# Optimization experiments

Measured on AMD Instinct MI355X. Metric: run time of the kernel, lower is better.

## Reference

```python
import jax, jax.numpy as jnp
import numpy as np

N = 40000      # total nodes in batched graph
E = 400000     # total edges
IN = 256       # input feature dim (n_dim / in_feats)
OUT = 256      # out_feats (DGL GatedGraphConv requires in_feats <= out_feats)
B = 256        # number of graphs in the batch
STEPS = 3      # GRU propagation steps per GatedGraphConv layer


def _gru_cell(m, h, Wih, Whh, bih, bhh):
    # torch.nn.GRUCell math
    gi = m @ Wih.T + bih          # [N, 3*OUT]
    gh = h @ Whh.T + bhh
    ir, iz, inn = jnp.split(gi, 3, axis=-1)
    hr, hz, hn = jnp.split(gh, 3, axis=-1)
    r = jax.nn.sigmoid(ir + hr)
    z = jax.nn.sigmoid(iz + hz)
    n = jnp.tanh(inn + r * hn)
    return (1.0 - z) * n + z * h


def _gated_graph_conv(h, src, dst, W, b, Wih, Whh, bih, bhh):
    # DGL GatedGraphConv with n_etypes=1: zero-pad to out_feats, then
    # n_steps of (per-etype linear -> sum messages over edges -> GRU update)
    if h.shape[1] < OUT:
        h = jnp.pad(h, ((0, 0), (0, OUT - h.shape[1])))
    for _ in range(STEPS):
        a = h @ W.T + b                                      # [N, OUT]
        m = jax.ops.segment_sum(a[src], dst, num_segments=N)  # gather/scatter
        h = _gru_cell(m, h, Wih, Whh, bih, bhh)
    return h


def _global_attention_pool(h, graph_ids, Wg, bg):
    gate = h @ Wg.T + bg                                       # [N, 1]
    gmax = jax.ops.segment_max(gate, graph_ids, num_segments=B)  # [B, 1]
    e = jnp.exp(gate - gmax[graph_ids])
    denom = jax.ops.segment_sum(e, graph_ids, num_segments=B)
    alpha = e / denom[graph_ids]                               # per-graph softmax
    return jax.ops.segment_sum(h * alpha, graph_ids, num_segments=B)  # [B, OUT]


def _forward(features, W0, b0, Wih0, Whh0, bih0, bhh0,
             W1, b1, Wih1, Whh1, bih1, bhh1, Wg, bg, Wo, bo,
             src, dst, graph_ids):
    # forward(): y = sigmoid(layer0(g, x)); y = sigmoid(layer1(g, y));
    # y = attention_pool(g, y); return sigmoid(output_layer(y))  (BCE branch)
    y = jax.nn.sigmoid(_gated_graph_conv(features, src, dst, W0, b0, Wih0, Whh0, bih0, bhh0))
    y = jax.nn.sigmoid(_gated_graph_conv(y, src, dst, W1, b1, Wih1, Whh1, bih1, bhh1))
    y = _global_attention_pool(y, graph_ids, Wg, bg)           # [B, OUT]
    return jax.nn.sigmoid(y @ Wo.T + bo)                        # [B, 1]


def setup_inputs() -> dict:
    key = jax.random.key(0)
    ks = jax.random.split(key, 20)
    s = lambda k, shape: (jax.random.normal(k, shape, jnp.float32) * 0.05)
    inp = {}
    inp["features"] = jax.random.normal(ks[0], (N, IN), jnp.float32)
    inp["src"] = jax.random.randint(ks[1], (E,), 0, N, jnp.int32)
    inp["dst"] = jax.random.randint(ks[2], (E,), 0, N, jnp.int32)
    inp["graph_ids"] = jnp.sort(jax.random.randint(ks[3], (N,), 0, B, jnp.int32))
    for li, off in ((0, 4), (1, 8)):
        inp[f"W{li}"] = s(ks[off], (OUT, OUT))
        inp[f"b{li}"] = jnp.zeros((OUT,), jnp.float32)
        inp[f"Wih{li}"] = s(ks[off + 1], (3 * OUT, OUT))
        inp[f"Whh{li}"] = s(ks[off + 2], (3 * OUT, OUT))
        inp[f"bih{li}"] = jnp.zeros((3 * OUT,), jnp.float32)
        inp[f"bhh{li}"] = jnp.zeros((3 * OUT,), jnp.float32)
    inp["Wg"] = s(ks[16], (1, OUT))
    inp["bg"] = jnp.zeros((1,), jnp.float32)
    inp["Wo"] = s(ks[17], (1, OUT))
    inp["bo"] = jnp.zeros((1,), jnp.float32)
    return inp


def reference(features, src, dst, graph_ids,
              W0, b0, Wih0, Whh0, bih0, bhh0,
              W1, b1, Wih1, Whh1, bih1, bhh1,
              Wg, bg, Wo, bo):
    return _forward(features, W0, b0, Wih0, Whh0, bih0, bhh0,
                    W1, b1, Wih1, Whh1, bih1, bhh1, Wg, bg, Wo, bo,
                    src, dst, graph_ids)
```

## Files before the change

### kernel.cpp

```cpp
#include <hip/hip_runtime.h>
#include <math.h>

#define NN 40000
#define EE 400000
#define BB 256

typedef __attribute__((ext_vector_type(8))) short short8;
typedef __attribute__((ext_vector_type(4))) float f32x4;
typedef __attribute__((address_space(1))) unsigned int glb_u32;
typedef __attribute__((address_space(3))) unsigned int lds_u32;

#define MFMA16 __builtin_amdgcn_mfma_f32_16x16x32_bf16

__device__ __forceinline__ float sigf(float x) { return 1.0f / (1.0f + __expf(-x)); }
__device__ __forceinline__ float tanhfast(float x) { return 2.0f / (1.0f + __expf(-2.0f * x)) - 1.0f; }
__device__ __forceinline__ unsigned short f2b(float f) {
    unsigned u = __float_as_uint(f);
    u += 0x7FFFu + ((u >> 16) & 1u);
    return (unsigned short)(u >> 16);
}
__device__ __forceinline__ float b2f(unsigned short h) { return __uint_as_float(((unsigned)h) << 16); }
__device__ __forceinline__ short8 ld8(const unsigned short* p) {
    return __builtin_bit_cast(short8, *(const uint4*)p);
}
__device__ __forceinline__ void gld_lds16(const void* g, void* l) {
    __builtin_amdgcn_global_load_lds((const glb_u32*)g, (lds_u32*)l, 16, 0, 0);
}

__global__ void k_f2b(const float* __restrict__ s, unsigned short* __restrict__ d, int n4) {
    int i = blockIdx.x * blockDim.x + threadIdx.x;
    if (i < n4) {
        float4 v = ((const float4*)s)[i];
        ushort4 o;
        o.x = f2b(v.x); o.y = f2b(v.y); o.z = f2b(v.z); o.w = f2b(v.w);
        ((ushort4*)d)[i] = o;
    }
}

__global__ __launch_bounds__(256) void k_wfuse(const float* __restrict__ Wih,
                                               const float* __restrict__ W,
                                               const float* __restrict__ b,
                                               unsigned short* __restrict__ Wf,
                                               float* __restrict__ vib) {
    int g = blockIdx.x;
    int c = threadIdx.x;
    __shared__ float row[256];
    __shared__ float red[256];
    row[c] = Wih[(size_t)g * 256 + c];
    __syncthreads();
    float acc = 0.f;
#pragma unroll 8
    for (int o = 0; o < 256; o++) acc += row[o] * W[(size_t)o * 256 + c];
    Wf[(size_t)g * 256 + c] = f2b(acc);
    red[c] = row[c] * b[c];
    __syncthreads();
    for (int off = 128; off; off >>= 1) {
        if (c < off) red[c] += red[c + off];
        __syncthreads();
    }
    if (c == 0) vib[g] = red[0];
}

__global__ void k_wpack(const unsigned short* __restrict__ Wf,
                        const float* __restrict__ Whh,
                        unsigned short* __restrict__ Wp) {
    int id = blockIdx.x * 256 + threadIdx.x;
    if (id >= 49152) return;
    int lane = id & 63;
    int t = (id >> 6) & 3;
    int q = (id >> 8) % 6;
    int bk = (id >> 8) / 6;
    int ks = bk & 7, bn_t = bk >> 3;
    int col = bn_t * 64 + t * 16 + (lane & 15);
    int k = ks * 32 + (lane >> 4) * 8;
    unsigned short o[8];
    if (q < 3) {
        const unsigned short* s = Wf + (size_t)(q * 256 + col) * 256 + k;
#pragma unroll
        for (int j = 0; j < 8; j++) o[j] = s[j];
    } else {
        const float* s = Whh + (size_t)((q - 3) * 256 + col) * 256 + k;
#pragma unroll
        for (int j = 0; j < 8; j++) o[j] = f2b(s[j]);
    }
    *(uint4*)(Wp + (size_t)id * 8) = *(const uint4*)o;
}

__global__ void k_zeroi(int* __restrict__ p, int n) {
    int i = blockIdx.x * blockDim.x + threadIdx.x;
    if (i < n) p[i] = 0;
}

__global__ void k_hist(const int* __restrict__ dst, int* __restrict__ cnt) {
    int e = blockIdx.x * blockDim.x + threadIdx.x;
    if (e < EE) atomicAdd(&cnt[dst[e]], 1);
}

__global__ __launch_bounds__(1024) void k_scanA(const int* __restrict__ cnt, int* __restrict__ rp,
                                                int* __restrict__ bsum) {
    __shared__ int sm[1024];
    int b = blockIdx.x, t = threadIdx.x;
    int i = b * 1024 + t;
    sm[t] = (i < NN) ? cnt[i] : 0;
    __syncthreads();
    for (int off = 1; off < 1024; off <<= 1) {
        int u = (t >= off) ? sm[t - off] : 0;
        __syncthreads();
        sm[t] += u;
        __syncthreads();
    }
    if (i < NN) rp[i + 1] = sm[t];
    if (t == 1023) bsum[b] = sm[1023];
}

__global__ void k_scanB(const int* __restrict__ bsum, int* __restrict__ boff, int* __restrict__ rp) {
    if (threadIdx.x == 0) {
        int run = 0;
        for (int k = 0; k < 40; k++) { boff[k] = run; run += bsum[k]; }
        rp[0] = 0;
    }
}

__global__ void k_scanC(int* __restrict__ rp, const int* __restrict__ boff) {
    int i = blockIdx.x * 256 + threadIdx.x;
    if (i < NN) rp[i + 1] += boff[i >> 10];
}

__global__ void k_fill(const int* __restrict__ src, const int* __restrict__ dst,
                       const int* __restrict__ rp, int* __restrict__ cur, int* __restrict__ cs) {
    int e = blockIdx.x * blockDim.x + threadIdx.x;
    if (e < EE) {
        int v = dst[e];
        int pos = rp[v] + atomicAdd(&cur[v], 1);
        cs[pos] = src[e];
    }
}

__device__ __forceinline__ void acc8(float* a, uint4 v) {
    a[0] += b2f((unsigned short)(v.x & 0xFFFF));
    a[1] += b2f((unsigned short)(v.x >> 16));
    a[2] += b2f((unsigned short)(v.y & 0xFFFF));
    a[3] += b2f((unsigned short)(v.y >> 16));
    a[4] += b2f((unsigned short)(v.z & 0xFFFF));
    a[5] += b2f((unsigned short)(v.z >> 16));
    a[6] += b2f((unsigned short)(v.w & 0xFFFF));
    a[7] += b2f((unsigned short)(v.w >> 16));
}

__global__ __launch_bounds__(256) void k_aggr(const unsigned short* __restrict__ Hb,
                                              const int* __restrict__ rp,
                                              const int* __restrict__ cs,
                                              unsigned short* __restrict__ Agg) {
    int v = blockIdx.x * 8 + (threadIdx.x >> 5);
    int hl = threadIdx.x & 31;
    int s = rp[v], e = rp[v + 1];
    float a[8] = {};
    int j = s;
    for (; j + 8 <= e; j += 8) {
        uint4 x0 = *(const uint4*)&Hb[(size_t)cs[j] * 256 + hl * 8];
        uint4 x1 = *(const uint4*)&Hb[(size_t)cs[j + 1] * 256 + hl * 8];
        uint4 x2 = *(const uint4*)&Hb[(size_t)cs[j + 2] * 256 + hl * 8];
        uint4 x3 = *(const uint4*)&Hb[(size_t)cs[j + 3] * 256 + hl * 8];
        uint4 x4 = *(const uint4*)&Hb[(size_t)cs[j + 4] * 256 + hl * 8];
        uint4 x5 = *(const uint4*)&Hb[(size_t)cs[j + 5] * 256 + hl * 8];
        uint4 x6 = *(const uint4*)&Hb[(size_t)cs[j + 6] * 256 + hl * 8];
        uint4 x7 = *(const uint4*)&Hb[(size_t)cs[j + 7] * 256 + hl * 8];
        acc8(a, x0); acc8(a, x1); acc8(a, x2); acc8(a, x3);
        acc8(a, x4); acc8(a, x5); acc8(a, x6); acc8(a, x7);
    }
    for (; j < e; j++) {
        uint4 x = *(const uint4*)&Hb[(size_t)cs[j] * 256 + hl * 8];
        acc8(a, x);
    }
    uint4 o;
    o.x = (unsigned)f2b(a[0]) | ((unsigned)f2b(a[1]) << 16);
    o.y = (unsigned)f2b(a[2]) | ((unsigned)f2b(a[3]) << 16);
    o.z = (unsigned)f2b(a[4]) | ((unsigned)f2b(a[5]) << 16);
    o.w = (unsigned)f2b(a[6]) | ((unsigned)f2b(a[7]) << 16);
    *(uint4*)&Agg[(size_t)v * 256 + hl * 8] = o;
}

__global__ __launch_bounds__(256, 3) void k_gru(const unsigned short* __restrict__ Mb,
                                                const unsigned short* __restrict__ Hb,
                                                const char* __restrict__ Wp,
                                                const float* __restrict__ bih,
                                                const float* __restrict__ bhh,
                                                const float* __restrict__ vib,
                                                const int* __restrict__ cnt,
                                                unsigned short* __restrict__ Hout, int fin) {
    __shared__ uint4 Wl[2][1536];
    const int tid = threadIdx.x;
    const int lane = tid & 63, wid = tid >> 6;
    const int wr = wid >> 1, wc = wid & 1;
    const int p = blockIdx.x;
    const int xcd = p & 7, rank = p >> 3;
    const int logical = (xcd < 4 ? xcd * 313 : 1252 + (xcd - 4) * 312) + rank;
    const int bm = (logical >> 2) * 64, bn_t = logical & 3, bn = bn_t * 64;
    const int l15 = lane & 15, lk = lane >> 4;

    const unsigned short* m0p = Mb + (size_t)(bm + wr * 32 + l15) * 256 + lk * 8;
    const unsigned short* m1p = m0p + 16 * 256;
    const unsigned short* h0p = Hb + (size_t)(bm + wr * 32 + l15) * 256 + lk * 8;
    const unsigned short* h1p = h0p + 16 * 256;

    const char* wbase = Wp + (size_t)bn_t * 8 * 24576;
    char* lds0 = (char*)&Wl[0][0];
    char* lds1 = (char*)&Wl[1][0];
    const int soff = wid * 1024 + lane * 16;

#define STAGE(b, ks)                                                        \
    {                                                                       \
        const char* gs = wbase + (ks) * 24576;                              \
        char* lb = (b) ? lds1 : lds0;                                       \
        _Pragma("unroll") for (int i = 0; i < 6; i++)                       \
            gld_lds16(gs + i * 4096 + soff, lb + i * 4096 + wid * 1024);    \
    }

    f32x4 acc[6][2][2] = {};
    short8 m0, m1, h0, h1, nm0, nm1, nh0, nh1;

    STAGE(0, 0);
    asm volatile("" ::: "memory");
    m0 = ld8(m0p); m1 = ld8(m1p); h0 = ld8(h0p); h1 = ld8(h1p);

    for (int ks = 0; ks < 8; ks++) {
        int cur = ks & 1;
        asm volatile("s_waitcnt vmcnt(4)" ::: "memory");
        __builtin_amdgcn_s_barrier();
        __builtin_amdgcn_sched_barrier(0);
        if (ks < 7) {
            STAGE(cur ^ 1, ks + 1);
            asm volatile("" ::: "memory");
            int ke = (ks + 1) * 32;
            nm0 = ld8(m0p + ke); nm1 = ld8(m1p + ke);
            nh0 = ld8(h0p + ke); nh1 = ld8(h1p + ke);
        }
        __builtin_amdgcn_s_setprio(1);
#pragma unroll
        for (int q = 0; q < 6; q++) {
            short8 b0 = __builtin_bit_cast(short8, Wl[cur][(q * 4 + wc * 2 + 0) * 64 + lane]);
            short8 b1 = __builtin_bit_cast(short8, Wl[cur][(q * 4 + wc * 2 + 1) * 64 + lane]);
            short8 a0 = q < 3 ? m0 : h0;
            short8 a1 = q < 3 ? m1 : h1;
            acc[q][0][0] = MFMA16(a0, b0, acc[q][0][0], 0, 0, 0);
            acc[q][1][0] = MFMA16(a1, b0, acc[q][1][0], 0, 0, 0);
            acc[q][0][1] = MFMA16(a0, b1, acc[q][0][1], 0, 0, 0);
            acc[q][1][1] = MFMA16(a1, b1, acc[q][1][1], 0, 0, 0);
        }
        __builtin_amdgcn_s_setprio(0);
        m0 = nm0; m1 = nm1; h0 = nh0; h1 = nh1;
    }
#undef STAGE

    const int lk4 = lk * 4;
#pragma unroll
    for (int f = 0; f < 2; f++)
#pragma unroll
        for (int t = 0; t < 2; t++) {
            int col = bn + wc * 32 + t * 16 + l15;
            float bi0 = bih[col], bi1 = bih[col + 256], bi2 = bih[col + 512];
            float bh0 = bhh[col], bh1 = bhh[col + 256], bh2 = bhh[col + 512];
            float v0 = vib[col], v1 = vib[col + 256], v2 = vib[col + 512];
#pragma unroll
            for (int r = 0; r < 4; r++) {
                int n = bm + wr * 32 + f * 16 + lk4 + r;
                float cf = (float)cnt[n];
                float ho = b2f(Hb[(size_t)n * 256 + col]);
                float irv = acc[0][f][t][r] + bi0 + cf * v0;
                float izv = acc[1][f][t][r] + bi1 + cf * v1;
                float inv = acc[2][f][t][r] + bi2 + cf * v2;
                float hrv = acc[3][f][t][r] + bh0;
                float hzv = acc[4][f][t][r] + bh1;
                float hnv = acc[5][f][t][r] + bh2;
                float rg = sigf(irv + hrv);
                float zg = sigf(izv + hzv);
                float nv = tanhfast(inv + rg * hnv);
                float v = (1.0f - zg) * nv + zg * ho;
                if (fin) v = sigf(v);
                Hout[(size_t)n * 256 + col] = f2b(v);
            }
        }
}

__global__ __launch_bounds__(256) void k_gate(const unsigned short* __restrict__ H,
                                              const float* __restrict__ Wg,
                                              const float* __restrict__ bg,
                                              float* __restrict__ gate) {
    int v = blockIdx.x * 4 + (threadIdx.x >> 6);
    int lane = threadIdx.x & 63;
    if (v >= NN) return;
    ushort4 hv = *(const ushort4*)&H[(size_t)v * 256 + lane * 4];
    float4 wv = *(const float4*)&Wg[lane * 4];
    float s = b2f(hv.x) * wv.x + b2f(hv.y) * wv.y + b2f(hv.z) * wv.z + b2f(hv.w) * wv.w;
    for (int off = 32; off; off >>= 1) s += __shfl_down(s, off);
    if (lane == 0) gate[v] = s + bg[0];
}

__global__ void k_bounds(const int* __restrict__ ids, int* __restrict__ gs, int* __restrict__ ge) {
    int b = threadIdx.x;
    int lo = 0, hi = NN;
    while (lo < hi) { int mid = (lo + hi) >> 1; if (ids[mid] < b) lo = mid + 1; else hi = mid; }
    gs[b] = lo;
    lo = 0; hi = NN;
    int key = b + 1;
    while (lo < hi) { int mid = (lo + hi) >> 1; if (ids[mid] < key) lo = mid + 1; else hi = mid; }
    ge[b] = lo;
}

__global__ __launch_bounds__(256) void k_pool(const unsigned short* __restrict__ H,
                                              const float* __restrict__ gate,
                                              const int* __restrict__ gs,
                                              const int* __restrict__ ge,
                                              float* __restrict__ pooled) {
    int b = blockIdx.x;
    int s = gs[b], e = ge[b];
    int t = threadIdx.x;
    __shared__ float red[256];
    __shared__ float wsh[256];
    float mx = -INFINITY;
    for (int n = s + t; n < e; n += 256) mx = fmaxf(mx, gate[n]);
    red[t] = mx;
    __syncthreads();
    for (int off = 128; off; off >>= 1) {
        if (t < off) red[t] = fmaxf(red[t], red[t + off]);
        __syncthreads();
    }
    mx = red[0];
    __syncthreads();
    float sm = 0.f;
    for (int n = s + t; n < e; n += 256) sm += __expf(gate[n] - mx);
    red[t] = sm;
    __syncthreads();
    for (int off = 128; off; off >>= 1) {
        if (t < off) red[t] += red[t + off];
        __syncthreads();
    }
    float denom = red[0];
    __syncthreads();
    float acc = 0.f;
    for (int c = s; c < e; c += 256) {
        int n = c + t;
        wsh[t] = (n < e) ? __expf(gate[n] - mx) / denom : 0.f;
        __syncthreads();
        int lim = e - c; if (lim > 256) lim = 256;
        for (int q = 0; q < lim; q++) acc += wsh[q] * b2f(H[(size_t)(c + q) * 256 + t]);
        __syncthreads();
    }
    pooled[(size_t)b * 256 + t] = acc;
}

__global__ void k_out(const float* __restrict__ pooled, const float* __restrict__ Wo,
                      const float* __restrict__ bo, float* __restrict__ out) {
    int b = blockIdx.x;
    int lane = threadIdx.x;
    float4 pv = *(const float4*)&pooled[(size_t)b * 256 + lane * 4];
    float4 wv = *(const float4*)&Wo[lane * 4];
    float s = pv.x * wv.x + pv.y * wv.y + pv.z * wv.z + pv.w * wv.w;
    for (int off = 32; off; off >>= 1) s += __shfl_down(s, off);
    if (lane == 0) out[b] = sigf(s + bo[0]);
}

extern "C" void kernel_launch(void* const* d_in, const int* in_sizes, int n_in,
                              void* d_out, int out_size, void* d_ws, size_t ws_size,
                              hipStream_t stream) {
    const float* features = (const float*)d_in[0];
    const int* src = (const int*)d_in[1];
    const int* dst = (const int*)d_in[2];
    const int* gids = (const int*)d_in[3];
    const float* W[2]   = {(const float*)d_in[4],  (const float*)d_in[10]};
    const float* bW[2]  = {(const float*)d_in[5],  (const float*)d_in[11]};
    const float* Wih[2] = {(const float*)d_in[6],  (const float*)d_in[12]};
    const float* Whh[2] = {(const float*)d_in[7],  (const float*)d_in[13]};
    const float* bih[2] = {(const float*)d_in[8],  (const float*)d_in[14]};
    const float* bhh[2] = {(const float*)d_in[9],  (const float*)d_in[15]};
    const float* Wg = (const float*)d_in[16];
    const float* bg = (const float*)d_in[17];
    const float* Wo = (const float*)d_in[18];
    const float* bo = (const float*)d_in[19];
    float* out = (float*)d_out;

    char* p = (char*)d_ws;
    auto alloc = [&](size_t bytes) {
        char* r = p;
        p += (bytes + 255) / 256 * 256;
        return r;
    };
    unsigned short* hbF = (unsigned short*)alloc((size_t)NN * 256 * 2);
    unsigned short* hA = (unsigned short*)alloc((size_t)NN * 256 * 2);
    unsigned short* hB = (unsigned short*)alloc((size_t)NN * 256 * 2);
    unsigned short* agg = (unsigned short*)alloc((size_t)NN * 256 * 2);
    unsigned short* Wfb[2], *Wpk[2];
    float* vib[2];
    for (int i = 0; i < 2; i++) {
        Wfb[i] = (unsigned short*)alloc((size_t)768 * 256 * 2);
        Wpk[i] = (unsigned short*)alloc((size_t)49152 * 16);
        vib[i] = (float*)alloc((size_t)768 * 4);
    }
    int* rp = (int*)alloc((size_t)(NN + 1) * 4);
    int* cnt = (int*)alloc((size_t)NN * 4);
    int* cur = (int*)alloc((size_t)NN * 4);
    int* cs = (int*)alloc((size_t)EE * 4);
    int* bsum = (int*)alloc(64 * 4);
    int* boff = (int*)alloc(64 * 4);
    float* gate = (float*)alloc((size_t)NN * 4);
    int* gsb = (int*)alloc((size_t)BB * 4);
    int* geb = (int*)alloc((size_t)BB * 4);
    float* pooled = (float*)alloc((size_t)BB * 256 * 4);

    k_f2b<<<(NN * 256 / 4 + 255) / 256, 256, 0, stream>>>(features, hbF, NN * 256 / 4);
    for (int i = 0; i < 2; i++) {
        k_wfuse<<<768, 256, 0, stream>>>(Wih[i], W[i], bW[i], Wfb[i], vib[i]);
        k_wpack<<<192, 256, 0, stream>>>(Wfb[i], Whh[i], Wpk[i]);
    }

    k_zeroi<<<(NN + 255) / 256, 256, 0, stream>>>(cnt, NN);
    k_zeroi<<<(NN + 255) / 256, 256, 0, stream>>>(cur, NN);
    k_hist<<<(EE + 255) / 256, 256, 0, stream>>>(dst, cnt);
    k_scanA<<<40, 1024, 0, stream>>>(cnt, rp, bsum);
    k_scanB<<<1, 64, 0, stream>>>(bsum, boff, rp);
    k_scanC<<<157, 256, 0, stream>>>(rp, boff);
    k_fill<<<(EE + 255) / 256, 256, 0, stream>>>(src, dst, rp, cur, cs);
    k_bounds<<<1, 256, 0, stream>>>(gids, gsb, geb);

    const unsigned short* hcur = hbF;
    unsigned short* hnext = hA;
    for (int li = 0; li < 2; li++) {
        for (int s = 0; s < 3; s++) {
            k_aggr<<<5000, 256, 0, stream>>>(hcur, rp, cs, agg);
            int fin = (s == 2) ? 1 : 0;
            k_gru<<<2500, 256, 0, stream>>>(agg, hcur, (const char*)Wpk[li], bih[li], bhh[li],
                                            vib[li], cnt, hnext, fin);
            hcur = hnext;
            hnext = (hnext == hA) ? hB : hA;
        }
    }
    k_gate<<<10000, 256, 0, stream>>>(hcur, Wg, bg, gate);
    k_pool<<<BB, 256, 0, stream>>>(hcur, gate, gsb, geb, pooled);
    k_out<<<BB, 64, 0, stream>>>(pooled, Wo, bo, out);
}
```

Baseline: 720.6 us.

## Triple-buffer GRU weight staging with two-stage-ahead prefetch

Converts the k_gru K-loop from a double-buffered to a triple-buffered pipeline. Weight tiles and M/H activation fragments are prefetched two k-steps ahead, with the vmcnt waits adjusted to match. The loop is fully unrolled so the register arrays index statically. This is meant to hide more global-load latency, but it raises LDS use per block to 72KB and lowers the launch-bounds occupancy hint from 3 to 2 blocks per CU.

```diff
diff --git a/kernel.cpp b/kernel.cpp
--- a/kernel.cpp
+++ b/kernel.cpp
@@ -180,7 +180,7 @@
     *(uint4*)&Agg[(size_t)v * 256 + hl * 8] = o;
 }
 
-__global__ __launch_bounds__(256, 3) void k_gru(const unsigned short* __restrict__ Mb,
+__global__ __launch_bounds__(256, 2) void k_gru(const unsigned short* __restrict__ Mb,
                                                 const unsigned short* __restrict__ Hb,
                                                 const char* __restrict__ Wp,
                                                 const float* __restrict__ bih,
@@ -188,7 +188,7 @@
                                                 const float* __restrict__ vib,
                                                 const int* __restrict__ cnt,
                                                 unsigned short* __restrict__ Hout, int fin) {
-    __shared__ uint4 Wl[2][1536];
+    __shared__ uint4 Wl[3][1536];
     const int tid = threadIdx.x;
     const int lane = tid & 63, wid = tid >> 6;
     const int wr = wid >> 1, wc = wid & 1;
@@ -204,51 +204,58 @@
     const unsigned short* h1p = h0p + 16 * 256;
 
     const char* wbase = Wp + (size_t)bn_t * 8 * 24576;
-    char* lds0 = (char*)&Wl[0][0];
-    char* lds1 = (char*)&Wl[1][0];
+    char* ldsb = (char*)&Wl[0][0];
     const int soff = wid * 1024 + lane * 16;
 
-#define STAGE(b, ks)                                                        \
+#define STAGE(bi, ks)                                                       \
     {                                                                       \
         const char* gs = wbase + (ks) * 24576;                              \
-        char* lb = (b) ? lds1 : lds0;                                       \
+        char* lb = ldsb + (bi) * 24576;                                     \
         _Pragma("unroll") for (int i = 0; i < 6; i++)                       \
             gld_lds16(gs + i * 4096 + soff, lb + i * 4096 + wid * 1024);    \
     }
 
     f32x4 acc[6][2][2] = {};
-    short8 m0, m1, h0, h1, nm0, nm1, nh0, nh1;
+    short8 m0[3], m1[3], h0[3], h1[3];
 
     STAGE(0, 0);
     asm volatile("" ::: "memory");
-    m0 = ld8(m0p); m1 = ld8(m1p); h0 = ld8(h0p); h1 = ld8(h1p);
-
+    m0[0] = ld8(m0p); m1[0] = ld8(m1p); h0[0] = ld8(h0p); h1[0] = ld8(h1p);
+    asm volatile("" ::: "memory");
+    STAGE(1, 1);
+    asm volatile("" ::: "memory");
+    m0[1] = ld8(m0p + 32); m1[1] = ld8(m1p + 32);
+    h0[1] = ld8(h0p + 32); h1[1] = ld8(h1p + 32);
+
+#pragma unroll
     for (int ks = 0; ks < 8; ks++) {
-        int cur = ks & 1;
-        asm volatile("s_waitcnt vmcnt(4)" ::: "memory");
+        const int cur = ks % 3;
+        if (ks < 7) asm volatile("s_waitcnt vmcnt(14)" ::: "memory");
+        else        asm volatile("s_waitcnt vmcnt(4)" ::: "memory");
         __builtin_amdgcn_s_barrier();
         __builtin_amdgcn_sched_barrier(0);
-        if (ks < 7) {
-            STAGE(cur ^ 1, ks + 1);
+        if (ks < 6) {
+            const int sl = (ks + 2) % 3;
+            STAGE(sl, ks + 2);
             asm volatile("" ::: "memory");
-            int ke = (ks + 1) * 32;
-            nm0 = ld8(m0p + ke); nm1 = ld8(m1p + ke);
-            nh0 = ld8(h0p + ke); nh1 = ld8(h1p + ke);
+            const int ke = (ks + 2) * 32;
+            m0[sl] = ld8(m0p + ke); m1[sl] = ld8(m1p + ke);
+            h0[sl] = ld8(h0p + ke); h1[sl] = ld8(h1p + ke);
+            asm volatile("" ::: "memory");
         }
         __builtin_amdgcn_s_setprio(1);
 #pragma unroll
         for (int q = 0; q < 6; q++) {
             short8 b0 = __builtin_bit_cast(short8, Wl[cur][(q * 4 + wc * 2 + 0) * 64 + lane]);
             short8 b1 = __builtin_bit_cast(short8, Wl[cur][(q * 4 + wc * 2 + 1) * 64 + lane]);
-            short8 a0 = q < 3 ? m0 : h0;
-            short8 a1 = q < 3 ? m1 : h1;
+            short8 a0 = q < 3 ? m0[cur] : h0[cur];
+            short8 a1 = q < 3 ? m1[cur] : h1[cur];
             acc[q][0][0] = MFMA16(a0, b0, acc[q][0][0], 0, 0, 0);
             acc[q][1][0] = MFMA16(a1, b0, acc[q][1][0], 0, 0, 0);
             acc[q][0][1] = MFMA16(a0, b1, acc[q][0][1], 0, 0, 0);
             acc[q][1][1] = MFMA16(a1, b1, acc[q][1][1], 0, 0, 0);
         }
         __builtin_amdgcn_s_setprio(0);
-        m0 = nm0; m1 = nm1; h0 = nh0; h1 = nh1;
     }
 #undef STAGE
 
```

Measured after the change: 768.1 us. +6.6%, slower.

## Halve GRU kernel column tile to 32 and double grid for higher occupancy

Applied to the files above, without the earlier changes.

The fused GRU GEMM kernel now computes a 64x32 output tile per block instead of 64x64. This halves the accumulators and the LDS weight staging buffer, raises launch bounds to 6 blocks per SM, and doubles the grid to 5000 blocks. The block-to-XCD remapping is simplified to match. The aim is more resident waves to hide memory latency, at the cost of loading the M and H A-operands twice as often across blocks.

```diff
diff --git a/kernel.cpp b/kernel.cpp
--- a/kernel.cpp
+++ b/kernel.cpp
@@ -180,7 +180,7 @@
     *(uint4*)&Agg[(size_t)v * 256 + hl * 8] = o;
 }
 
-__global__ __launch_bounds__(256, 3) void k_gru(const unsigned short* __restrict__ Mb,
+__global__ __launch_bounds__(256, 6) void k_gru(const unsigned short* __restrict__ Mb,
                                                 const unsigned short* __restrict__ Hb,
                                                 const char* __restrict__ Wp,
                                                 const float* __restrict__ bih,
@@ -188,14 +188,15 @@
                                                 const float* __restrict__ vib,
                                                 const int* __restrict__ cnt,
                                                 unsigned short* __restrict__ Hout, int fin) {
-    __shared__ uint4 Wl[2][1536];
+    __shared__ uint4 Wl[2][768];
     const int tid = threadIdx.x;
     const int lane = tid & 63, wid = tid >> 6;
     const int wr = wid >> 1, wc = wid & 1;
     const int p = blockIdx.x;
-    const int xcd = p & 7, rank = p >> 3;
-    const int logical = (xcd < 4 ? xcd * 313 : 1252 + (xcd - 4) * 312) + rank;
-    const int bm = (logical >> 2) * 64, bn_t = logical & 3, bn = bn_t * 64;
+    const int logical = (p & 7) * 625 + (p >> 3);
+    const int rowtile = logical >> 3, bn32 = logical & 7;
+    const int bm = rowtile * 64;
+    const int bn_t = bn32 >> 1, hw = bn32 & 1;
     const int l15 = lane & 15, lk = lane >> 4;
 
     const unsigned short* m0p = Mb + (size_t)(bm + wr * 32 + l15) * 256 + lk * 8;
@@ -203,83 +204,80 @@
     const unsigned short* h0p = Hb + (size_t)(bm + wr * 32 + l15) * 256 + lk * 8;
     const unsigned short* h1p = h0p + 16 * 256;
 
-    const char* wbase = Wp + (size_t)bn_t * 8 * 24576;
+    const char* wbase = Wp + (size_t)bn_t * 196608 + hw * 2048 + lane * 16;
     char* lds0 = (char*)&Wl[0][0];
-    char* lds1 = (char*)&Wl[1][0];
-    const int soff = wid * 1024 + lane * 16;
-
-#define STAGE(b, ks)                                                        \
-    {                                                                       \
-        const char* gs = wbase + (ks) * 24576;                              \
-        char* lb = (b) ? lds1 : lds0;                                       \
-        _Pragma("unroll") for (int i = 0; i < 6; i++)                       \
-            gld_lds16(gs + i * 4096 + soff, lb + i * 4096 + wid * 1024);    \
-    }
-
-    f32x4 acc[6][2][2] = {};
-    short8 m0, m1, h0, h1, nm0, nm1, nh0, nh1;
+
+#define STAGE(b, ks)                                                          \
+    {                                                                         \
+        const char* gs = wbase + (ks) * 24576;                                \
+        char* lb = lds0 + (b) * 12288;                                        \
+        _Pragma("unroll") for (int i = 0; i < 3; i++) {                       \
+            int f = wid * 3 + i;                                              \
+            gld_lds16(gs + (f >> 1) * 4096 + (f & 1) * 1024, lb + f * 1024);  \
+        }                                                                     \
+    }
+
+    f32x4 acc[6][2] = {};
+    short8 am0, am1, ah0, ah1, nm0, nm1, nh0, nh1;
 
     STAGE(0, 0);
     asm volatile("" ::: "memory");
-    m0 = ld8(m0p); m1 = ld8(m1p); h0 = ld8(h0p); h1 = ld8(h1p);
-
+    am0 = ld8(m0p); am1 = ld8(m1p); ah0 = ld8(h0p); ah1 = ld8(h1p);
+
+#pragma unroll
     for (int ks = 0; ks < 8; ks++) {
-        int cur = ks & 1;
+        const int cur = ks & 1;
         asm volatile("s_waitcnt vmcnt(4)" ::: "memory");
         __builtin_amdgcn_s_barrier();
         __builtin_amdgcn_sched_barrier(0);
         if (ks < 7) {
             STAGE(cur ^ 1, ks + 1);
             asm volatile("" ::: "memory");
-            int ke = (ks + 1) * 32;
+            const int ke = (ks + 1) * 32;
             nm0 = ld8(m0p + ke); nm1 = ld8(m1p + ke);
             nh0 = ld8(h0p + ke); nh1 = ld8(h1p + ke);
+            asm volatile("" ::: "memory");
         }
         __builtin_amdgcn_s_setprio(1);
 #pragma unroll
         for (int q = 0; q < 6; q++) {
-            short8 b0 = __builtin_bit_cast(short8, Wl[cur][(q * 4 + wc * 2 + 0) * 64 + lane]);
-            short8 b1 = __builtin_bit_cast(short8, Wl[cur][(q * 4 + wc * 2 + 1) * 64 + lane]);
-            short8 a0 = q < 3 ? m0 : h0;
-            short8 a1 = q < 3 ? m1 : h1;
-            acc[q][0][0] = MFMA16(a0, b0, acc[q][0][0], 0, 0, 0);
-            acc[q][1][0] = MFMA16(a1, b0, acc[q][1][0], 0, 0, 0);
-            acc[q][0][1] = MFMA16(a0, b1, acc[q][0][1], 0, 0, 0);
-            acc[q][1][1] = MFMA16(a1, b1, acc[q][1][1], 0, 0, 0);
+            short8 b = __builtin_bit_cast(short8, Wl[cur][(q * 2 + wc) * 64 + lane]);
+            short8 a0 = q < 3 ? am0 : ah0;
+            short8 a1 = q < 3 ? am1 : ah1;
+            acc[q][0] = MFMA16(a0, b, acc[q][0], 0, 0, 0);
+            acc[q][1] = MFMA16(a1, b, acc[q][1], 0, 0, 0);
         }
         __builtin_amdgcn_s_setprio(0);
-        m0 = nm0; m1 = nm1; h0 = nh0; h1 = nh1;
+        am0 = nm0; am1 = nm1; ah0 = nh0; ah1 = nh1;
     }
 #undef STAGE
 
     const int lk4 = lk * 4;
-#pragma unroll
-    for (int f = 0; f < 2; f++)
-#pragma unroll
-        for (int t = 0; t < 2; t++) {
-            int col = bn + wc * 32 + t * 16 + l15;
-            float bi0 = bih[col], bi1 = bih[col + 256], bi2 = bih[col + 512];
-            float bh0 = bhh[col], bh1 = bhh[col + 256], bh2 = bhh[col + 512];
-            float v0 = vib[col], v1 = vib[col + 256], v2 = vib[col + 512];
-#pragma unroll
-            for (int r = 0; r < 4; r++) {
-                int n = bm + wr * 32 + f * 16 + lk4 + r;
-                float cf = (float)cnt[n];
-                float ho = b2f(Hb[(size_t)n * 256 + col]);
-                float irv = acc[0][f][t][r] + bi0 + cf * v0;
-                float izv = acc[1][f][t][r] + bi1 + cf * v1;
-                float inv = acc[2][f][t][r] + bi2 + cf * v2;
-                float hrv = acc[3][f][t][r] + bh0;
-                float hzv = acc[4][f][t][r] + bh1;
-                float hnv = acc[5][f][t][r] + bh2;
-                float rg = sigf(irv + hrv);
-                float zg = sigf(izv + hzv);
-                float nv = tanhfast(inv + rg * hnv);
-                float v = (1.0f - zg) * nv + zg * ho;
-                if (fin) v = sigf(v);
-                Hout[(size_t)n * 256 + col] = f2b(v);
-            }
+    const int col = bn_t * 64 + hw * 32 + wc * 16 + l15;
+    float bi0 = bih[col], bi1 = bih[col + 256], bi2 = bih[col + 512];
+    float bh0 = bhh[col], bh1 = bhh[col + 256], bh2 = bhh[col + 512];
+    float v0 = vib[col], v1 = vib[col + 256], v2 = vib[col + 512];
+#pragma unroll
+    for (int f = 0; f < 2; f++) {
+#pragma unroll
+        for (int r = 0; r < 4; r++) {
+            int n = bm + wr * 32 + f * 16 + lk4 + r;
+            float cf = (float)cnt[n];
+            float ho = b2f(Hb[(size_t)n * 256 + col]);
+            float irv = acc[0][f][r] + bi0 + cf * v0;
+            float izv = acc[1][f][r] + bi1 + cf * v1;
+            float inv = acc[2][f][r] + bi2 + cf * v2;
+            float hrv = acc[3][f][r] + bh0;
+            float hzv = acc[4][f][r] + bh1;
+            float hnv = acc[5][f][r] + bh2;
+            float rg = sigf(irv + hrv);
+            float zg = sigf(izv + hzv);
+            float nv = tanhfast(inv + rg * hnv);
+            float v = (1.0f - zg) * nv + zg * ho;
+            if (fin) v = sigf(v);
+            Hout[(size_t)n * 256 + col] = f2b(v);
         }
+    }
 }
 
 __global__ __launch_bounds__(256) void k_gate(const unsigned short* __restrict__ H,
@@ -428,7 +426,7 @@
         for (int s = 0; s < 3; s++) {
             k_aggr<<<5000, 256, 0, stream>>>(hcur, rp, cs, agg);
             int fin = (s == 2) ? 1 : 0;
-            k_gru<<<2500, 256, 0, stream>>>(agg, hcur, (const char*)Wpk[li], bih[li], bhh[li],
+            k_gru<<<5000, 256, 0, stream>>>(agg, hcur, (const char*)Wpk[li], bih[li], bhh[li],
                                             vib[li], cnt, hnext, fin);
             hcur = hnext;
             hnext = (hnext == hA) ? hB : hA;
```

After: 2.513 ms. 249% more time.

## Enlarge GRU GEMM tile to 128 rows with 512-thread blocks sharing weight LDS

Applied to the files above, without the earlier changes.

The fused GRU GEMM kernel now uses 512-thread blocks covering 128 node rows instead of 64. The double-buffered weight tile staged into LDS is shared by twice as many rows, so each block issues half as many global-to-LDS copies per row of output. The grid shrinks to 1252 blocks with remapped XCD assignment, and bounds checks are added for the padded last tile. Occupancy drops to two blocks per CU, and more waves must synchronise at each barrier.

```diff
diff --git a/kernel.cpp b/kernel.cpp
--- a/kernel.cpp
+++ b/kernel.cpp
@@ -180,7 +180,7 @@
     *(uint4*)&Agg[(size_t)v * 256 + hl * 8] = o;
 }
 
-__global__ __launch_bounds__(256, 3) void k_gru(const unsigned short* __restrict__ Mb,
+__global__ __launch_bounds__(512, 2) void k_gru(const unsigned short* __restrict__ Mb,
                                                 const unsigned short* __restrict__ Hb,
                                                 const char* __restrict__ Wp,
                                                 const float* __restrict__ bih,
@@ -191,29 +191,30 @@
     __shared__ uint4 Wl[2][1536];
     const int tid = threadIdx.x;
     const int lane = tid & 63, wid = tid >> 6;
-    const int wr = wid >> 1, wc = wid & 1;
+    const int rt = wid >> 2, wr = (wid >> 1) & 1, wc = wid & 1;
     const int p = blockIdx.x;
     const int xcd = p & 7, rank = p >> 3;
-    const int logical = (xcd < 4 ? xcd * 313 : 1252 + (xcd - 4) * 312) + rank;
-    const int bm = (logical >> 2) * 64, bn_t = logical & 3, bn = bn_t * 64;
+    const int logical = (xcd < 4 ? xcd * 157 : 628 + (xcd - 4) * 156) + rank;
+    const int bm = (logical >> 2) * 128, bn_t = logical & 3, bn = bn_t * 64;
     const int l15 = lane & 15, lk = lane >> 4;
 
-    const unsigned short* m0p = Mb + (size_t)(bm + wr * 32 + l15) * 256 + lk * 8;
-    const unsigned short* m1p = m0p + 16 * 256;
-    const unsigned short* h0p = Hb + (size_t)(bm + wr * 32 + l15) * 256 + lk * 8;
-    const unsigned short* h1p = h0p + 16 * 256;
-
-    const char* wbase = Wp + (size_t)bn_t * 8 * 24576;
+    const int rbase = bm + rt * 64 + wr * 32 + l15;
+    const int rA = (rbase < NN) ? rbase : 0;
+    const int rB = (rbase + 16 < NN) ? rbase + 16 : 0;
+    const unsigned short* m0p = Mb + (size_t)rA * 256 + lk * 8;
+    const unsigned short* m1p = Mb + (size_t)rB * 256 + lk * 8;
+    const unsigned short* h0p = Hb + (size_t)rA * 256 + lk * 8;
+    const unsigned short* h1p = Hb + (size_t)rB * 256 + lk * 8;
+
+    const char* wbase = Wp + (size_t)bn_t * 196608 + wid * 3072 + lane * 16;
     char* lds0 = (char*)&Wl[0][0];
-    char* lds1 = (char*)&Wl[1][0];
-    const int soff = wid * 1024 + lane * 16;
-
-#define STAGE(b, ks)                                                        \
-    {                                                                       \
-        const char* gs = wbase + (ks) * 24576;                              \
-        char* lb = (b) ? lds1 : lds0;                                       \
-        _Pragma("unroll") for (int i = 0; i < 6; i++)                       \
-            gld_lds16(gs + i * 4096 + soff, lb + i * 4096 + wid * 1024);    \
+
+#define STAGE(b, ks)                                              \
+    {                                                             \
+        const char* gs = wbase + (ks) * 24576;                    \
+        char* lb = lds0 + (b) * 24576 + wid * 3072;               \
+        _Pragma("unroll") for (int i = 0; i < 3; i++)             \
+            gld_lds16(gs + i * 1024, lb + i * 1024);              \
     }
 
     f32x4 acc[6][2][2] = {};
@@ -223,17 +224,19 @@
     asm volatile("" ::: "memory");
     m0 = ld8(m0p); m1 = ld8(m1p); h0 = ld8(h0p); h1 = ld8(h1p);
 
+#pragma unroll
     for (int ks = 0; ks < 8; ks++) {
-        int cur = ks & 1;
+        const int cur = ks & 1;
         asm volatile("s_waitcnt vmcnt(4)" ::: "memory");
         __builtin_amdgcn_s_barrier();
         __builtin_amdgcn_sched_barrier(0);
         if (ks < 7) {
             STAGE(cur ^ 1, ks + 1);
             asm volatile("" ::: "memory");
-            int ke = (ks + 1) * 32;
+            const int ke = (ks + 1) * 32;
             nm0 = ld8(m0p + ke); nm1 = ld8(m1p + ke);
             nh0 = ld8(h0p + ke); nh1 = ld8(h1p + ke);
+            asm volatile("" ::: "memory");
         }
         __builtin_amdgcn_s_setprio(1);
 #pragma unroll
@@ -263,21 +266,23 @@
             float v0 = vib[col], v1 = vib[col + 256], v2 = vib[col + 512];
 #pragma unroll
             for (int r = 0; r < 4; r++) {
-                int n = bm + wr * 32 + f * 16 + lk4 + r;
-                float cf = (float)cnt[n];
-                float ho = b2f(Hb[(size_t)n * 256 + col]);
-                float irv = acc[0][f][t][r] + bi0 + cf * v0;
-                float izv = acc[1][f][t][r] + bi1 + cf * v1;
-                float inv = acc[2][f][t][r] + bi2 + cf * v2;
-                float hrv = acc[3][f][t][r] + bh0;
-                float hzv = acc[4][f][t][r] + bh1;
-                float hnv = acc[5][f][t][r] + bh2;
-                float rg = sigf(irv + hrv);
-                float zg = sigf(izv + hzv);
-                float nv = tanhfast(inv + rg * hnv);
-                float v = (1.0f - zg) * nv + zg * ho;
-                if (fin) v = sigf(v);
-                Hout[(size_t)n * 256 + col] = f2b(v);
+                int n = bm + rt * 64 + wr * 32 + f * 16 + lk4 + r;
+                if (n < NN) {
+                    float cf = (float)cnt[n];
+                    float ho = b2f(Hb[(size_t)n * 256 + col]);
+                    float irv = acc[0][f][t][r] + bi0 + cf * v0;
+                    float izv = acc[1][f][t][r] + bi1 + cf * v1;
+                    float inv = acc[2][f][t][r] + bi2 + cf * v2;
+                    float hrv = acc[3][f][t][r] + bh0;
+                    float hzv = acc[4][f][t][r] + bh1;
+                    float hnv = acc[5][f][t][r] + bh2;
+                    float rg = sigf(irv + hrv);
+                    float zg = sigf(izv + hzv);
+                    float nv = tanhfast(inv + rg * hnv);
+                    float v = (1.0f - zg) * nv + zg * ho;
+                    if (fin) v = sigf(v);
+                    Hout[(size_t)n * 256 + col] = f2b(v);
+                }
             }
         }
 }
@@ -428,7 +433,7 @@
         for (int s = 0; s < 3; s++) {
             k_aggr<<<5000, 256, 0, stream>>>(hcur, rp, cs, agg);
             int fin = (s == 2) ? 1 : 0;
-            k_gru<<<2500, 256, 0, stream>>>(agg, hcur, (const char*)Wpk[li], bih[li], bhh[li],
+            k_gru<<<1252, 512, 0, stream>>>(agg, hcur, (const char*)Wpk[li], bih[li], bhh[li],
                                             vib[li], cnt, hnext, fin);
             hcur = hnext;
             hnext = (hnext == hA) ? hB : hA;
```

Result: slower. 803.6 us (+11.5%).
